# Optimization experiments

Hardware: AMD Instinct MI355X
Metric: run time of the kernel (lower is better)

Reference implementation:

```python
import jax, jax.numpy as jnp
import numpy as np

FS = 3          # filter_size
B, C, H, W = 16, 256, 96, 96
BN_EPS = 1e-5


def setup_inputs() -> dict:
    key = jax.random.key(0)
    ks = jax.random.split(key, 6)
    s = 0.05
    return {
        "x": jax.random.normal(ks[0], (B, C, H, W), jnp.float32),
        "convoluted": jax.random.normal(ks[1], (B, C, H, W), jnp.float32),
        # filter_gen_conv: 1x1 Conv2d(C -> C)
        "w_gen": jax.random.normal(ks[2], (C, C, 1, 1), jnp.float32) * s,
        "b_gen": jax.random.normal(ks[3], (C,), jnp.float32) * s,
        # c1: 3x3 Conv2d(C -> C) + BatchNorm2d(C) + ReLU
        "w_c1": jax.random.normal(ks[4], (C, C, 3, 3), jnp.float32) * s,
        "b_c1": jax.random.normal(ks[5], (C,), jnp.float32) * s,
        "gamma": jnp.ones((C,), jnp.float32),
        "beta": jnp.zeros((C,), jnp.float32),
    }


def reference(x, convoluted, w_gen, b_gen, w_c1, b_c1, gamma, beta):
    b, c, h, w = x.shape
    # adaptive_avg_pool2d(x, FS): H,W divisible by FS -> uniform bins
    pooled = x.reshape(b, c, FS, h // FS, FS, w // FS).mean(axis=(3, 5))  # [b,c,FS,FS]
    # 1x1 conv generating per-sample per-channel filters
    gen = jnp.einsum('bcij,oc->boij', pooled, w_gen[:, :, 0, 0]) + b_gen[None, :, None, None]

    # c1: conv3x3 (pad 1) + BatchNorm (training-mode batch stats) + ReLU
    y = jax.lax.conv_general_dilated(
        convoluted, w_c1, window_strides=(1, 1), padding=((1, 1), (1, 1)),
        dimension_numbers=('NCHW', 'OIHW', 'NCHW')) + b_c1[None, :, None, None]
    mu = y.mean(axis=(0, 2, 3), keepdims=True)
    var = y.var(axis=(0, 2, 3), keepdims=True)
    y = (y - mu) * jax.lax.rsqrt(var + BN_EPS)
    y = jax.nn.relu(y * gamma[None, :, None, None] + beta[None, :, None, None])

    # dynamic per-sample depthwise conv: groups = b*c, symmetric pad (FS odd)
    y = y.reshape(1, b * c, h, w)
    filt = gen.reshape(b * c, 1, FS, FS)
    pad = (FS - 1) // 2
    out = jax.lax.conv_general_dilated(
        y, filt, window_strides=(1, 1), padding=((pad, pad), (pad, pad)),
        feature_group_count=b * c, dimension_numbers=('NCHW', 'OIHW', 'NCHW'))
    return out.reshape(b, c, h, w)
```

## Files before the change

kernel.cpp:

```cpp
#include <hip/hip_runtime.h>

typedef __bf16 bf16x8 __attribute__((ext_vector_type(8)));
typedef float f32x4 __attribute__((ext_vector_type(4)));

static __device__ __forceinline__ ushort f2b(float f) {
    uint32_t x = __float_as_uint(f);
    x += 0x7fffu + ((x >> 16) & 1u);
    return (ushort)(x >> 16);
}
static __device__ __forceinline__ float b2f(ushort u) {
    return __uint_as_float(((uint32_t)u) << 16);
}

typedef const __attribute__((address_space(1))) uint32_t gu32;
typedef __attribute__((address_space(3))) uint32_t lu32;
static __device__ __forceinline__ void gl_lds16(const void* g, void* l) {
    __builtin_amdgcn_global_load_lds((gu32*)g, (lu32*)l, 16, 0, 0);
}

__global__ __launch_bounds__(256) void pool_k(const float* __restrict__ x,
                                              float* __restrict__ pooled) {
    const int bc  = blockIdx.x;
    const int tid = threadIdx.x;
    const int lane = tid & 63, wv = tid >> 6;
    const float4* p4 = (const float4*)(x + (size_t)bc * 9216);
    __shared__ float red[4][9];
#pragma unroll
    for (int bi = 0; bi < 3; ++bi) {
#pragma unroll
        for (int bj = 0; bj < 3; ++bj) {
            int row = bi * 32 + (tid >> 3);
            int c4  = bj * 8 + (tid & 7);
            float4 f = p4[row * 24 + c4];
            float s = f.x + f.y + f.z + f.w;
#pragma unroll
            for (int off = 32; off; off >>= 1) s += __shfl_down(s, off);
            if (lane == 0) red[wv][bi * 3 + bj] = s;
        }
    }
    __syncthreads();
    if (tid < 9) {
        float s = red[0][tid] + red[1][tid] + red[2][tid] + red[3][tid];
        pooled[(size_t)bc * 9 + tid] = s * (1.0f / 1024.0f);
    }
}

__global__ __launch_bounds__(256) void gen_k(const float* __restrict__ pooled,
                                             const float* __restrict__ wgen,
                                             const float* __restrict__ bgen,
                                             float* __restrict__ gen) {
    __shared__ float pl[256];
    const int b = blockIdx.x / 9, ij = blockIdx.x % 9;
    const int o = threadIdx.x;
    pl[o] = pooled[((size_t)b * 256 + o) * 9 + ij];
    __syncthreads();
    float a = bgen[o];
    const float4* wg4 = (const float4*)(wgen + (size_t)o * 256);
    const float4* pl4 = (const float4*)pl;
#pragma unroll 4
    for (int q = 0; q < 64; ++q) {
        float4 w = wg4[q], p = pl4[q];
        a += w.x * p.x + w.y * p.y + w.z * p.z + w.w * p.w;
    }
    gen[((size_t)b * 256 + o) * 9 + ij] = a;
}

__global__ __launch_bounds__(256) void wtr_k(const float* __restrict__ wc1,
                                             ushort* __restrict__ wtr) {
    int g = blockIdx.x * 256 + threadIdx.x;
    int step = g >> 10;
    int row  = (g >> 2) & 255;
    int c8   = g & 3;
    int ch = step / 9, tap = step - ch * 9;
    int cb = ch * 32 + c8 * 8;
    ushort tmp[8];
#pragma unroll
    for (int j = 0; j < 8; ++j)
        tmp[j] = f2b(wc1[(size_t)row * 2304 + (size_t)(cb + j) * 9 + tap]);
    *(uint4*)(wtr + (size_t)g * 8) = *(const uint4*)tmp;
}

__global__ __launch_bounds__(512) void xt_k(const float* __restrict__ xin,
                                            ushort* __restrict__ xt,
                                            ushort* __restrict__ zeros) {
    __shared__ ushort T[96][258];
    const int bh = blockIdx.x;
    const int b = bh / 96, h = bh % 96;
    const int tid = threadIdx.x;
    const float* src = xin + (size_t)b * 2359296 + (size_t)h * 96;
#pragma unroll
    for (int it = 0; it < 12; ++it) {
        int id = tid + it * 512;
        int c = id / 24, q = id - c * 24;
        float4 v = *(const float4*)(src + (size_t)c * 9216 + q * 4);
        int px = q * 4;
        T[px + 0][c] = f2b(v.x); T[px + 1][c] = f2b(v.y);
        T[px + 2][c] = f2b(v.z); T[px + 3][c] = f2b(v.w);
    }
    __syncthreads();
    ushort* dst = xt + (size_t)bh * 24576;
#pragma unroll
    for (int it = 0; it < 12; ++it) {
        int id = tid + it * 512;
        int px = id >> 6, cq = id & 63;
        ushort4 u;
        u.x = T[px][cq * 4 + 0]; u.y = T[px][cq * 4 + 1];
        u.z = T[px][cq * 4 + 2]; u.w = T[px][cq * 4 + 3];
        *(ushort4*)(dst + px * 256 + cq * 4) = u;
    }
    if (bh == 0 && tid < 512) zeros[tid] = 0;
}

__global__ __launch_bounds__(512) void conv_k(const ushort* __restrict__ xt,
                                              const ushort* __restrict__ wtr,
                                              const float* __restrict__ bc1,
                                              const ushort* __restrict__ zeros,
                                              ushort* __restrict__ yb,
                                              float* __restrict__ part) {
    __shared__ ushort Bl[2][12544];

    const int blk0 = blockIdx.x;
    const int blk = (blk0 & 7) * 96 + (blk0 >> 3);
    const int b = blk / 48, hg = blk % 48, h0 = hg * 2;
    const int tid = threadIdx.x;
    const int lane = tid & 63, wv = tid >> 6;
    const int wm = wv & 3, wn = wv >> 2;
    const int lo = lane & 15, hi = lane >> 4;

    {
        int bsel = tid >> 8, rem = tid & 255;
        int row = rem >> 6, pxp = ((rem >> 5) & 1) ? 97 : 0, c = rem & 31;
        Bl[bsel][(row * 98 + pxp) * 32 + c] = 0;
    }

    const ushort* ssrc[3];
    int sdst[3];
    bool sval[3];
#pragma unroll
    for (int j = 0; j < 3; ++j) {
        int s = wv * 3 + j, row = s / 6, pseg = s - row * 6;
        int r = h0 + row - 1;
        sval[j] = ((unsigned)r < 96u);
        ssrc[j] = sval[j]
            ? (xt + (((size_t)(b * 96 + r) * 96 + pseg * 16 + (lane >> 2)) * 256
                     + (lane & 3) * 8))
            : (zeros + lane * 8);
        sdst[j] = (row * 98 + 1 + pseg * 16) * 32;
    }

    const uint4* Abase = (const uint4*)wtr + ((wm * 64 + lo) * 4 + hi);

    f32x4 acc[4][6] = {};
    uint4 abuf[2][4];

#pragma unroll
    for (int j = 0; j < 3; ++j)
        gl_lds16(ssrc[j], &Bl[0][sdst[j]]);
#pragma unroll
    for (int mi = 0; mi < 4; ++mi) abuf[0][mi] = Abase[mi * 64];
    __syncthreads();

    for (int k = 0; k < 4; ++k) {
#pragma unroll
        for (int t = 0; t < 18; ++t) {
            const int cur = t & 1;
            if (t == 0) {
#pragma unroll
                for (int j = 0; j < 3; ++j)
                    gl_lds16(ssrc[j] + (sval[j] ? (2 * k + 1) * 32 : 0),
                             &Bl[1][sdst[j]]);
            } else if (t == 9 && k < 3) {
#pragma unroll
                for (int j = 0; j < 3; ++j)
                    gl_lds16(ssrc[j] + (sval[j] ? (2 * k + 2) * 32 : 0),
                             &Bl[0][sdst[j]]);
            }
            if (t < 17 || k < 3) {
                const uint4* Ap = Abase + (size_t)(k * 18 + t + 1) * 1024;
#pragma unroll
                for (int mi = 0; mi < 4; ++mi) abuf[cur ^ 1][mi] = Ap[mi * 64];
            }
            const int tap = (t < 9) ? t : t - 9;
            const int dy = tap / 3, dx = tap % 3;
            const ushort* Bp =
                &Bl[t >= 9][((wn + dy) * 98 + lo + dx) * 32 + hi * 8];
            bf16x8 bfr[6];
#pragma unroll
            for (int ni = 0; ni < 6; ++ni)
                bfr[ni] = *(const bf16x8*)(Bp + ni * 512);
#pragma unroll
            for (int mi = 0; mi < 4; ++mi) {
                const bf16x8 af = *(const bf16x8*)&abuf[cur][mi];
#pragma unroll
                for (int ni = 0; ni < 6; ++ni)
                    acc[mi][ni] = __builtin_amdgcn_mfma_f32_16x16x32_bf16(
                        af, bfr[ni], acc[mi][ni], 0, 0, 0);
            }
            if (t == 8) __syncthreads();
            else if (t == 17 && k < 3) __syncthreads();
        }
    }

    const size_t ybase = (size_t)(b * 96 + h0 + wn) * 24576;
#pragma unroll
    for (int mi = 0; mi < 4; ++mi) {
        float s[4], s2[4];
#pragma unroll
        for (int rr = 0; rr < 4; ++rr) {
            const int o = wm * 64 + mi * 16 + hi * 4 + rr;
            const float bias = bc1[o];
            float sv = 0.f, sv2 = 0.f;
#pragma unroll
            for (int ni = 0; ni < 6; ++ni) {
                const int px = ni * 16 + lo;
                float v = acc[mi][ni][rr] + bias;
                yb[ybase + o * 96 + px] = f2b(v);
                sv += v; sv2 += v * v;
            }
            s[rr] = sv; s2[rr] = sv2;
        }
#pragma unroll
        for (int off = 1; off < 16; off <<= 1) {
#pragma unroll
            for (int rr = 0; rr < 4; ++rr) {
                s[rr]  += __shfl_xor(s[rr], off);
                s2[rr] += __shfl_xor(s2[rr], off);
            }
        }
        if (lo == 0) {
#pragma unroll
            for (int rr = 0; rr < 4; ++rr) {
                const int o = wm * 64 + mi * 16 + hi * 4 + rr;
                part[(size_t)o * 1536 + blk * 2 + wn]          = s[rr];
                part[393216 + (size_t)o * 1536 + blk * 2 + wn] = s2[rr];
            }
        }
    }
}

__global__ __launch_bounds__(256) void bnred_k(const float* __restrict__ part,
                                               const float* __restrict__ gamma,
                                               const float* __restrict__ beta,
                                               float* __restrict__ bnp) {
    const int o = blockIdx.x, t = threadIdx.x;
    const float* p0 = part + (size_t)o * 1536;
    const float* p1 = p0 + 393216;
    float s = 0.f, s2 = 0.f;
#pragma unroll
    for (int k = 0; k < 6; ++k) { s += p0[t + k * 256]; s2 += p1[t + k * 256]; }
    const int lane = t & 63, wv = t >> 6;
#pragma unroll
    for (int off = 32; off; off >>= 1) {
        s  += __shfl_down(s, off);
        s2 += __shfl_down(s2, off);
    }
    __shared__ float r1[4], r2[4];
    if (lane == 0) { r1[wv] = s; r2[wv] = s2; }
    __syncthreads();
    if (t == 0) {
        float S  = r1[0] + r1[1] + r1[2] + r1[3];
        float S2 = r2[0] + r2[1] + r2[2] + r2[3];
        const float invN = 1.0f / 147456.0f;
        float mu  = S * invN;
        float var = S2 * invN - mu * mu;
        float sc  = gamma[o] * rsqrtf(var + 1e-5f);
        bnp[o]       = sc;
        bnp[256 + o] = beta[o] - mu * sc;
    }
}

__global__ __launch_bounds__(256) void dw_k(const ushort* __restrict__ yb,
                                            const float* __restrict__ gen,
                                            const float* __restrict__ bnp,
                                            float* __restrict__ out) {
    __shared__ float pl[9216];
    const int bc = blockIdx.x, tid = threadIdx.x;
    const int b = bc >> 8, c = bc & 255;
    const float sc = bnp[c], sh = bnp[256 + c];
    const ushort4* yb4 = (const ushort4*)yb;
    const size_t pbase = (size_t)b * 589824 + c * 24;
#pragma unroll
    for (int it = 0; it < 9; ++it) {
        int e4 = tid + it * 256;
        int row = e4 / 24, px4 = e4 - row * 24;
        ushort4 u = yb4[pbase + (size_t)row * 6144 + px4];
        float4 f;
        f.x = fmaxf(b2f(u.x) * sc + sh, 0.f);
        f.y = fmaxf(b2f(u.y) * sc + sh, 0.f);
        f.z = fmaxf(b2f(u.z) * sc + sh, 0.f);
        f.w = fmaxf(b2f(u.w) * sc + sh, 0.f);
        *(float4*)&pl[e4 * 4] = f;
    }
    float g[9];
    const float* gp = gen + (size_t)bc * 9;
#pragma unroll
    for (int k = 0; k < 9; ++k) g[k] = gp[k];
    __syncthreads();
    float* op = out + (size_t)bc * 9216;
#pragma unroll
    for (int it = 0; it < 36; ++it) {
        int i = tid + it * 256;
        int row = i / 96, col = i - row * 96;
        float a = 0.f;
#pragma unroll
        for (int dy = 0; dy < 3; ++dy) {
            int rr = row + dy - 1;
            if (rr < 0 || rr >= 96) continue;
#pragma unroll
            for (int dxq = 0; dxq < 3; ++dxq) {
                int cc = col + dxq - 1;
                if (cc < 0 || cc >= 96) continue;
                a += pl[rr * 96 + cc] * g[dy * 3 + dxq];
            }
        }
        op[i] = a;
    }
}

extern "C" void kernel_launch(void* const* d_in, const int* in_sizes, int n_in,
                              void* d_out, int out_size, void* d_ws, size_t ws_size,
                              hipStream_t stream) {
    const float* x       = (const float*)d_in[0];
    const float* conv_in = (const float*)d_in[1];
    const float* w_gen   = (const float*)d_in[2];
    const float* b_gen   = (const float*)d_in[3];
    const float* w_c1    = (const float*)d_in[4];
    const float* b_c1    = (const float*)d_in[5];
    const float* gamma   = (const float*)d_in[6];
    const float* beta    = (const float*)d_in[7];
    float* out = (float*)d_out;

    char* ws = (char*)d_ws;
    float*  pooled = (float*)(ws + 0);
    float*  gen    = (float*)(ws + 147456);
    ushort* wtr    = (ushort*)(ws + 294912);
    float*  part   = (float*)(ws + 1474560);
    float*  bnp    = (float*)(ws + 4620288);
    ushort* zeros  = (ushort*)(ws + 4622336);
    ushort* yb     = (ushort*)(ws + 4624384);
    ushort* xt     = (ushort*)d_out;

    pool_k <<<4096, 256, 0, stream>>>(x, pooled);
    gen_k  <<<144,  256, 0, stream>>>(pooled, w_gen, b_gen, gen);
    wtr_k  <<<288,  256, 0, stream>>>(w_c1, wtr);
    xt_k   <<<1536, 512, 0, stream>>>(conv_in, xt, zeros);
    conv_k <<<768,  512, 0, stream>>>(xt, wtr, b_c1, zeros, yb, part);
    bnred_k<<<256,  256, 0, stream>>>(part, gamma, beta, bnp);
    dw_k   <<<4096, 256, 0, stream>>>(yb, gen, bnp, out);
}
```

Before: 389.6 us.

## Shrink conv tile to one output row per 256-thread block

The 3x3 conv kernel now computes one output row per block with 4 waves instead of two rows with 8 waves, doubling the grid to 1536 blocks and cutting the LDS halo buffer from 4 to 3 input rows. Each wave still covers 64 output channels by 96 pixels. The aim is more resident blocks per CU and better load balance across CUs. The cost is that each block reuses its halo less (3 staged rows per output row instead of 2), and the total weight traffic doubles.

```diff
diff --git a/kernel.cpp b/kernel.cpp
--- a/kernel.cpp
+++ b/kernel.cpp
@@ -111,36 +111,42 @@
     if (bh == 0 && tid < 512) zeros[tid] = 0;
 }
 
-__global__ __launch_bounds__(512) void conv_k(const ushort* __restrict__ xt,
+__global__ __launch_bounds__(256) void conv_k(const ushort* __restrict__ xt,
                                               const ushort* __restrict__ wtr,
                                               const float* __restrict__ bc1,
                                               const ushort* __restrict__ zeros,
                                               ushort* __restrict__ yb,
                                               float* __restrict__ part) {
-    __shared__ ushort Bl[2][12544];
+    __shared__ ushort Bl[2][9408];
 
     const int blk0 = blockIdx.x;
-    const int blk = (blk0 & 7) * 96 + (blk0 >> 3);
-    const int b = blk / 48, hg = blk % 48, h0 = hg * 2;
+    const int blk = (blk0 & 7) * 192 + (blk0 >> 3);
+    const int b = blk / 96, h = blk % 96;
     const int tid = threadIdx.x;
     const int lane = tid & 63, wv = tid >> 6;
-    const int wm = wv & 3, wn = wv >> 2;
     const int lo = lane & 15, hi = lane >> 4;
 
-    {
-        int bsel = tid >> 8, rem = tid & 255;
-        int row = rem >> 6, pxp = ((rem >> 5) & 1) ? 97 : 0, c = rem & 31;
-        Bl[bsel][(row * 98 + pxp) * 32 + c] = 0;
-    }
-
-    const ushort* ssrc[3];
-    int sdst[3];
-    bool sval[3];
-#pragma unroll
-    for (int j = 0; j < 3; ++j) {
-        int s = wv * 3 + j, row = s / 6, pseg = s - row * 6;
-        int r = h0 + row - 1;
-        sval[j] = ((unsigned)r < 96u);
+#pragma unroll
+    for (int z0 = 0; z0 < 2; ++z0) {
+        int z = tid + z0 * 256;
+        if (z < 384) {
+            int bsel = z >= 192, rem = z - bsel * 192;
+            int row = rem >> 6, pxp = ((rem >> 5) & 1) ? 97 : 0, c = rem & 31;
+            Bl[bsel][(row * 98 + pxp) * 32 + c] = 0;
+        }
+    }
+
+    const ushort* ssrc[5];
+    int sdst[5];
+    bool sact[5], sval[5];
+#pragma unroll
+    for (int j = 0; j < 5; ++j) {
+        int s = wv + j * 4;
+        sact[j] = (s < 18);
+        int sc = sact[j] ? s : 0;
+        int row = sc / 6, pseg = sc - row * 6;
+        int r = h + row - 1;
+        sval[j] = sact[j] && ((unsigned)r < 96u);
         ssrc[j] = sval[j]
             ? (xt + (((size_t)(b * 96 + r) * 96 + pseg * 16 + (lane >> 2)) * 256
                      + (lane & 3) * 8))
@@ -148,14 +154,14 @@
         sdst[j] = (row * 98 + 1 + pseg * 16) * 32;
     }
 
-    const uint4* Abase = (const uint4*)wtr + ((wm * 64 + lo) * 4 + hi);
+    const uint4* Abase = (const uint4*)wtr + ((wv * 64 + lo) * 4 + hi);
 
     f32x4 acc[4][6] = {};
     uint4 abuf[2][4];
 
 #pragma unroll
-    for (int j = 0; j < 3; ++j)
-        gl_lds16(ssrc[j], &Bl[0][sdst[j]]);
+    for (int j = 0; j < 5; ++j)
+        if (sact[j]) gl_lds16(ssrc[j], &Bl[0][sdst[j]]);
 #pragma unroll
     for (int mi = 0; mi < 4; ++mi) abuf[0][mi] = Abase[mi * 64];
     __syncthreads();
@@ -166,14 +172,16 @@
             const int cur = t & 1;
             if (t == 0) {
 #pragma unroll
-                for (int j = 0; j < 3; ++j)
-                    gl_lds16(ssrc[j] + (sval[j] ? (2 * k + 1) * 32 : 0),
-                             &Bl[1][sdst[j]]);
+                for (int j = 0; j < 5; ++j)
+                    if (sact[j])
+                        gl_lds16(ssrc[j] + (sval[j] ? (2 * k + 1) * 32 : 0),
+                                 &Bl[1][sdst[j]]);
             } else if (t == 9 && k < 3) {
 #pragma unroll
-                for (int j = 0; j < 3; ++j)
-                    gl_lds16(ssrc[j] + (sval[j] ? (2 * k + 2) * 32 : 0),
-                             &Bl[0][sdst[j]]);
+                for (int j = 0; j < 5; ++j)
+                    if (sact[j])
+                        gl_lds16(ssrc[j] + (sval[j] ? (2 * k + 2) * 32 : 0),
+                                 &Bl[0][sdst[j]]);
             }
             if (t < 17 || k < 3) {
                 const uint4* Ap = Abase + (size_t)(k * 18 + t + 1) * 1024;
@@ -182,8 +190,7 @@
             }
             const int tap = (t < 9) ? t : t - 9;
             const int dy = tap / 3, dx = tap % 3;
-            const ushort* Bp =
-                &Bl[t >= 9][((wn + dy) * 98 + lo + dx) * 32 + hi * 8];
+            const ushort* Bp = &Bl[t >= 9][(dy * 98 + lo + dx) * 32 + hi * 8];
             bf16x8 bfr[6];
 #pragma unroll
             for (int ni = 0; ni < 6; ++ni)
@@ -201,13 +208,13 @@
         }
     }
 
-    const size_t ybase = (size_t)(b * 96 + h0 + wn) * 24576;
+    const size_t ybase = (size_t)blk * 24576;
 #pragma unroll
     for (int mi = 0; mi < 4; ++mi) {
         float s[4], s2[4];
 #pragma unroll
         for (int rr = 0; rr < 4; ++rr) {
-            const int o = wm * 64 + mi * 16 + hi * 4 + rr;
+            const int o = wv * 64 + mi * 16 + hi * 4 + rr;
             const float bias = bc1[o];
             float sv = 0.f, sv2 = 0.f;
 #pragma unroll
@@ -230,9 +237,9 @@
         if (lo == 0) {
 #pragma unroll
             for (int rr = 0; rr < 4; ++rr) {
-                const int o = wm * 64 + mi * 16 + hi * 4 + rr;
-                part[(size_t)o * 1536 + blk * 2 + wn]          = s[rr];
-                part[393216 + (size_t)o * 1536 + blk * 2 + wn] = s2[rr];
+                const int o = wv * 64 + mi * 16 + hi * 4 + rr;
+                part[(size_t)o * 1536 + blk]          = s[rr];
+                part[393216 + (size_t)o * 1536 + blk] = s2[rr];
             }
         }
     }
@@ -344,7 +351,7 @@
     gen_k  <<<144,  256, 0, stream>>>(pooled, w_gen, b_gen, gen);
     wtr_k  <<<288,  256, 0, stream>>>(w_c1, wtr);
     xt_k   <<<1536, 512, 0, stream>>>(conv_in, xt, zeros);
-    conv_k <<<768,  512, 0, stream>>>(xt, wtr, b_c1, zeros, yb, part);
+    conv_k <<<1536, 256, 0, stream>>>(xt, wtr, b_c1, zeros, yb, part);
     bnred_k<<<256,  256, 0, stream>>>(part, gamma, beta, bnp);
     dw_k   <<<4096, 256, 0, stream>>>(yb, gen, bnp, out);
 }
```

New measurement: 490.0 us. +25.8%, slower.
